# Kernel tuning notes

Hardware: AMD Instinct MI355X
Metric: run time of the kernel (lower is better)

The kernel has to match this reference:

```python
import jax, jax.numpy as jnp
import numpy as np


def setup_inputs() -> dict:
    key = jax.random.key(0)
    k1, k2 = jax.random.split(key)
    pred = jax.random.normal(k1, (8, 4096, 2), dtype=jnp.float32)
    target = jax.random.normal(k2, (8, 4096, 2), dtype=jnp.float32)
    return {"pred": pred, "target": target}


def reference(pred, target):
    # pred: [B, N, D], target: [B, M, D]
    # pairwise euclidean distances per batch: [B, N, M]
    diff = pred[:, :, None, :] - target[:, None, :, :]  # [B, N, M, D]
    dist = jnp.sqrt(jnp.sum(diff * diff, axis=-1))       # [B, N, M]
    # directed Hausdorff h(a,b) = max_i min_j d(a_i, b_j)
    h_ab = jnp.max(jnp.min(dist, axis=2), axis=1)        # [B]
    h_ba = jnp.max(jnp.min(dist, axis=1), axis=1)        # [B]
    score = jnp.maximum(h_ab, h_ba)                      # symmetric Hausdorff per batch
    return jnp.mean(score)
```

## Files before the change

kernel.cpp:

```cpp
#include <hip/hip_runtime.h>
#include <hip/hip_bf16.h>
#include <math.h>


#define B 8
#define N 4096
#define TPB 256
#define IB 8
#define JC 32
#define JTILE (N / JC)
#define ITILES (N / TPB)

typedef float v2f __attribute__((ext_vector_type(2)));

__global__ __launch_bounds__(TPB) void hk_partial(const float* __restrict__ pred,
                                                  const float* __restrict__ target,
                                                  float* __restrict__ pw) {
    const int bx  = blockIdx.x;
    const int ib  = bx & 1;
    const int jc  = bx >> 1;
    const int b   = blockIdx.y;
    const int dir = blockIdx.z;

    const float2* __restrict__ P =
        reinterpret_cast<const float2*>(dir == 0 ? pred : target) + (size_t)b * N;
    const float*  __restrict__ Qf =
        (dir == 0 ? target : pred) + (size_t)b * N * 2 + (size_t)jc * JTILE * 2;

    __shared__ float4 sQ[JTILE / 2];
    if (threadIdx.x < JTILE / 2)
        sQ[threadIdx.x] = reinterpret_cast<const float4*>(Qf)[threadIdx.x];
    __syncthreads();

    v2f m2x[IB], m2y[IB];
    float pp[IB], mn[IB];
    const int i0 = ib * (TPB * IB) + threadIdx.x;
    #pragma unroll
    for (int k = 0; k < IB; ++k) {
        float2 p = P[i0 + k * TPB];
        float ax = -2.f * p.x, ay = -2.f * p.y;
        m2x[k] = (v2f){ax, ax};
        m2y[k] = (v2f){ay, ay};
        pp[k]  = fmaf(p.x, p.x, p.y * p.y);
        mn[k]  = 3.402823466e38f;
    }

    #pragma unroll 4
    for (int j = 0; j < JTILE / 2; ++j) {
        float4 q = sQ[j];
        v2f qx = (v2f){q.x, q.z};
        v2f qy = (v2f){q.y, q.w};
        v2f qq = __builtin_elementwise_fma(qx, qx, qy * qy);
        #pragma unroll
        for (int k = 0; k < IB; ++k) {
            v2f t = __builtin_elementwise_fma(m2y[k], qy, qq);
            t     = __builtin_elementwise_fma(m2x[k], qx, t);
            mn[k] = fminf(mn[k], fminf(t.x, t.y));
        }
    }

    float* dst = pw + (size_t)((dir * B + b) * JC + jc) * N;
    #pragma unroll
    for (int k = 0; k < IB; ++k)
        dst[i0 + k * TPB] = mn[k] + pp[k];
}

__global__ __launch_bounds__(TPB) void hk_maxred(const float* __restrict__ pw,
                                                 float* __restrict__ pw2) {
    const int tile = blockIdx.x;
    const int b    = blockIdx.y;
    const int dir  = blockIdx.z;
    const int t    = threadIdx.x;

    const float* base = pw + (size_t)((dir * B + b) * JC) * N + tile * TPB + t;
    float mnv = base[0];
    #pragma unroll
    for (int jc = 1; jc < JC; ++jc) mnv = fminf(mnv, base[(size_t)jc * N]);

    float mx = mnv;
    #pragma unroll
    for (int off = 32; off > 0; off >>= 1)
        mx = fmaxf(mx, __shfl_down(mx, off, 64));

    __shared__ float sred[TPB / 64];
    if ((t & 63) == 0) sred[t >> 6] = mx;
    __syncthreads();
    if (t == 0) {
        float bm = sred[0];
        #pragma unroll
        for (int w = 1; w < TPB / 64; ++w) bm = fmaxf(bm, sred[w]);
        pw2[(dir * B + b) * ITILES + tile] = bm;
    }
}

__global__ __launch_bounds__(64) void hk_final(const float* __restrict__ pw2,
                                               float* __restrict__ out) {
    const int t = threadIdx.x;
    __shared__ float h2[2 * B];
    if (t < 2 * B) {
        float mx = pw2[t * ITILES];
        #pragma unroll
        for (int k = 1; k < ITILES; ++k) mx = fmaxf(mx, pw2[t * ITILES + k]);
        h2[t] = mx;
    }
    __syncthreads();
    if (t == 0) {
        float s = 0.f;
        #pragma unroll
        for (int b = 0; b < B; ++b)
            s += sqrtf(fmaxf(fmaxf(h2[b], h2[B + b]), 0.f));
        out[0] = s * (1.0f / B);
    }
}

extern "C" void kernel_launch(void* const* d_in, const int* in_sizes, int n_in,
                              void* d_out, int out_size, void* d_ws, size_t ws_size,
                              hipStream_t stream) {
    const float* pred   = (const float*)d_in[0];
    const float* target = (const float*)d_in[1];
    float* out = (float*)d_out;
    float* pw  = (float*)d_ws;
    float* pw2 = (float*)((char*)d_ws + (size_t)2 * B * JC * N * sizeof(float));

    dim3 g1(64, B, 2);
    hk_partial<<<g1, TPB, 0, stream>>>(pred, target, pw);
    dim3 g2(ITILES, B, 2);
    hk_maxred<<<g2, TPB, 0, stream>>>(pw, pw2);
    hk_final<<<1, 64, 0, stream>>>(pw2, out);
}
```

Baseline: 80.05 us.

## Raise per-thread i-blocking, split j finer, fuse final reduction via atomics

The partial kernel now gives each thread 16 query points instead of 8 and splits the target set into 64 chunks instead of 32. Each block then covers all 4096 rows for its chunk, so total block count stays at 1024. The LDS layout is swizzled so x and y pairs load directly as vectors. The third kernel is removed: the max-reduction kernel does an atomicMax on the float bits per (dir, batch) and uses a last-block counter to compute the final mean. This adds a memset launch and doubles the partial-min workspace traffic. The float-as-int atomicMax is only valid because squared distances are non-negative.

```diff
diff --git a/kernel.cpp b/kernel.cpp
--- a/kernel.cpp
+++ b/kernel.cpp
@@ -6,21 +6,21 @@
 #define B 8
 #define N 4096
 #define TPB 256
-#define IB 8
-#define JC 32
+#define IB 16
+#define JC 64
 #define JTILE (N / JC)
 #define ITILES (N / TPB)
+#define RBLOCKS (ITILES * B * 2)
 
 typedef float v2f __attribute__((ext_vector_type(2)));
 
-__global__ __launch_bounds__(TPB) void hk_partial(const float* __restrict__ pred,
-                                                  const float* __restrict__ target,
-                                                  float* __restrict__ pw) {
-    const int bx  = blockIdx.x;
-    const int ib  = bx & 1;
-    const int jc  = bx >> 1;
+__global__ __launch_bounds__(TPB, 4) void hk_partial(const float* __restrict__ pred,
+                                                     const float* __restrict__ target,
+                                                     float* __restrict__ pw) {
+    const int jc  = blockIdx.x;
     const int b   = blockIdx.y;
     const int dir = blockIdx.z;
+    const int t   = threadIdx.x;
 
     const float2* __restrict__ P =
         reinterpret_cast<const float2*>(dir == 0 ? pred : target) + (size_t)b * N;
@@ -28,16 +28,17 @@
         (dir == 0 ? target : pred) + (size_t)b * N * 2 + (size_t)jc * JTILE * 2;
 
     __shared__ float4 sQ[JTILE / 2];
-    if (threadIdx.x < JTILE / 2)
-        sQ[threadIdx.x] = reinterpret_cast<const float4*>(Qf)[threadIdx.x];
+    if (t < JTILE / 2) {
+        float4 g = reinterpret_cast<const float4*>(Qf)[t];
+        sQ[t] = make_float4(g.x, g.z, g.y, g.w);
+    }
     __syncthreads();
 
     v2f m2x[IB], m2y[IB];
     float pp[IB], mn[IB];
-    const int i0 = ib * (TPB * IB) + threadIdx.x;
     #pragma unroll
     for (int k = 0; k < IB; ++k) {
-        float2 p = P[i0 + k * TPB];
+        float2 p = P[t + k * TPB];
         float ax = -2.f * p.x, ay = -2.f * p.y;
         m2x[k] = (v2f){ax, ax};
         m2y[k] = (v2f){ay, ay};
@@ -45,28 +46,30 @@
         mn[k]  = 3.402823466e38f;
     }
 
-    #pragma unroll 4
+    #pragma unroll 2
     for (int j = 0; j < JTILE / 2; ++j) {
-        float4 q = sQ[j];
-        v2f qx = (v2f){q.x, q.z};
-        v2f qy = (v2f){q.y, q.w};
+        float4 qv = sQ[j];
+        v2f qx = (v2f){qv.x, qv.y};
+        v2f qy = (v2f){qv.z, qv.w};
         v2f qq = __builtin_elementwise_fma(qx, qx, qy * qy);
         #pragma unroll
         for (int k = 0; k < IB; ++k) {
-            v2f t = __builtin_elementwise_fma(m2y[k], qy, qq);
-            t     = __builtin_elementwise_fma(m2x[k], qx, t);
-            mn[k] = fminf(mn[k], fminf(t.x, t.y));
+            v2f s = __builtin_elementwise_fma(m2y[k], qy, qq);
+            s     = __builtin_elementwise_fma(m2x[k], qx, s);
+            mn[k] = fminf(mn[k], fminf(s.x, s.y));
         }
     }
 
     float* dst = pw + (size_t)((dir * B + b) * JC + jc) * N;
     #pragma unroll
     for (int k = 0; k < IB; ++k)
-        dst[i0 + k * TPB] = mn[k] + pp[k];
+        dst[t + k * TPB] = mn[k] + pp[k];
 }
 
 __global__ __launch_bounds__(TPB) void hk_maxred(const float* __restrict__ pw,
-                                                 float* __restrict__ pw2) {
+                                                 int* __restrict__ slots,
+                                                 int* __restrict__ cnt,
+                                                 float* __restrict__ out) {
     const int tile = blockIdx.x;
     const int b    = blockIdx.y;
     const int dir  = blockIdx.z;
@@ -83,32 +86,30 @@
         mx = fmaxf(mx, __shfl_down(mx, off, 64));
 
     __shared__ float sred[TPB / 64];
+    __shared__ int sflag;
     if ((t & 63) == 0) sred[t >> 6] = mx;
     __syncthreads();
     if (t == 0) {
         float bm = sred[0];
         #pragma unroll
         for (int w = 1; w < TPB / 64; ++w) bm = fmaxf(bm, sred[w]);
-        pw2[(dir * B + b) * ITILES + tile] = bm;
+        atomicMax(&slots[dir * B + b], __float_as_int(bm));
+        __threadfence();
+        int old = atomicAdd(cnt, 1);
+        sflag = (old == RBLOCKS - 1);
     }
-}
+    __syncthreads();
+    if (!sflag) return;
 
-__global__ __launch_bounds__(64) void hk_final(const float* __restrict__ pw2,
-                                               float* __restrict__ out) {
-    const int t = threadIdx.x;
-    __shared__ float h2[2 * B];
-    if (t < 2 * B) {
-        float mx = pw2[t * ITILES];
-        #pragma unroll
-        for (int k = 1; k < ITILES; ++k) mx = fmaxf(mx, pw2[t * ITILES + k]);
-        h2[t] = mx;
-    }
+    __threadfence();
+    __shared__ float sh2[2 * B];
+    if (t < 2 * B) sh2[t] = __int_as_float(atomicMax(&slots[t], 0));
     __syncthreads();
     if (t == 0) {
         float s = 0.f;
         #pragma unroll
-        for (int b = 0; b < B; ++b)
-            s += sqrtf(fmaxf(fmaxf(h2[b], h2[B + b]), 0.f));
+        for (int bb = 0; bb < B; ++bb)
+            s += sqrtf(fmaxf(fmaxf(sh2[bb], sh2[B + bb]), 0.f));
         out[0] = s * (1.0f / B);
     }
 }
@@ -119,12 +120,15 @@
     const float* pred   = (const float*)d_in[0];
     const float* target = (const float*)d_in[1];
     float* out = (float*)d_out;
-    float* pw  = (float*)d_ws;
-    float* pw2 = (float*)((char*)d_ws + (size_t)2 * B * JC * N * sizeof(float));
 
-    dim3 g1(64, B, 2);
+    int*   slots = (int*)d_ws;
+    int*   cnt   = (int*)d_ws + 16;
+    float* pw    = (float*)((char*)d_ws + 256);
+
+    hipMemsetAsync(d_ws, 0, 128, stream);
+
+    dim3 g1(JC, B, 2);
     hk_partial<<<g1, TPB, 0, stream>>>(pred, target, pw);
     dim3 g2(ITILES, B, 2);
-    hk_maxred<<<g2, TPB, 0, stream>>>(pw, pw2);
-    hk_final<<<1, 64, 0, stream>>>(pw2, out);
+    hk_maxred<<<g2, TPB, 0, stream>>>(pw, slots, cnt, out);
 }
```

New measurement: 98.42 us. +22.9%, slower.
